# Optimization experiments

Hardware: AMD Instinct MI355X
Metric: run time of the kernel (lower is better)

The kernel has to match this reference:

```python
import jax, jax.numpy as jnp
import numpy as np

N = 50000      # num_nodes
E = 800000     # undirected edge count (maps holds 2E directed maps)
D = 4          # stalk dimension


def setup_inputs() -> dict:
    key = jax.random.key(0)
    k1, k2, k3 = jax.random.split(key, 3)
    maps = jax.random.normal(k1, (2 * E, D, D), dtype=jnp.float32) * 0.3
    # ensure every node appears as a source at least once (avoids degenerate
    # identity eigenproblems for isolated nodes)
    row = jnp.concatenate([jnp.arange(N, dtype=jnp.int32),
                           jax.random.randint(k2, (E - N,), 0, N, dtype=jnp.int32)])
    col = jax.random.randint(k3, (E,), 0, N, dtype=jnp.int32)
    # second half of edge_index is the reversed orientation, as the module assumes
    edge_index = jnp.stack([jnp.concatenate([row, col]),
                            jnp.concatenate([col, row])])
    return {"maps": maps, "edge_index": edge_index, "num_nodes": N}


def reference(maps, edge_index, num_nodes):
    n = num_nodes
    d = maps.shape[1]
    twoE = maps.shape[0]
    Ee = twoE // 2
    row_all = edge_index[0]                                   # [2E]
    # diag contribution: R^T R per directed edge, scatter-added onto source node
    diag_contrib = jnp.einsum('eki,ekj->eij', maps, maps)     # [2E,d,d]
    maps_diag = jnp.zeros((n, d, d), maps.dtype).at[row_all].add(diag_contrib)
    row = edge_index[0, :Ee]
    col = edge_index[1, :Ee]
    # off-diagonal block: R_ij^T R_ji per undirected edge
    maps_triu = jnp.einsum('eki,ekj->eij', maps[:Ee], maps[Ee:])  # [E,d,d]
    # eval-mode augmentation: + I
    to_inv = maps_diag + jnp.eye(d, dtype=maps.dtype)
    evals, evecs = jnp.linalg.eigh(to_inv)                    # batched tiny eigh
    inv_sqrt = jnp.einsum('nik,nk,njk->nij', evecs,
                          jnp.clip(evals, 1e-8, None) ** -0.5, evecs)
    # normalize: D^{-1/2} blocks, clamp to [-1, 1]
    maps_triu = jnp.clip(jnp.einsum('eik,ekl,elj->eij',
                                    inv_sqrt[row], maps_triu, inv_sqrt[col]), -1.0, 1.0)
    maps_diag = jnp.clip(jnp.einsum('nik,nkl,nlj->nij',
                                    inv_sqrt, maps_diag, inv_sqrt), -1.0, 1.0)
    # COO assembly of the (n*d, n*d) sheaf Laplacian
    ar = jnp.arange(d, dtype=jnp.int32)
    A, B = jnp.meshgrid(ar, ar, indexing='ij')                # [d,d]
    node = jnp.arange(n, dtype=jnp.int32)
    diag_rows = (node[:, None, None] * d + A).reshape(-1)
    diag_cols = (node[:, None, None] * d + B).reshape(-1)
    tri_rows_ij = (row[:, None, None] * d + A).reshape(-1)
    tri_cols_ij = (col[:, None, None] * d + B).reshape(-1)
    tri_rows_ji = (col[:, None, None] * d + A).reshape(-1)
    tri_cols_ji = (row[:, None, None] * d + B).reshape(-1)
    rows = jnp.concatenate([diag_rows, tri_rows_ij, tri_rows_ji])
    cols = jnp.concatenate([diag_cols, tri_cols_ij, tri_cols_ji])
    vals = jnp.concatenate([maps_diag.reshape(-1),
                            (-maps_triu).reshape(-1),
                            (-jnp.swapaxes(maps_triu, 1, 2)).reshape(-1)])
    indices = jnp.stack([rows, cols])                         # [2, K]
    return indices, vals
```

## Files before the change

kernel.cpp:

```cpp
#include <hip/hip_runtime.h>

#define DEG_CAP 96

__device__ __forceinline__ void load4x4(const float* __restrict__ p, float m[4][4]) {
    const float4* q = (const float4*)p;
#pragma unroll
    for (int k = 0; k < 4; ++k) {
        float4 v = q[k];
        m[k][0] = v.x; m[k][1] = v.y; m[k][2] = v.z; m[k][3] = v.w;
    }
}

__device__ __forceinline__ void store4x4(float* __restrict__ p, const float m[4][4]) {
    float4* q = (float4*)p;
#pragma unroll
    for (int k = 0; k < 4; ++k)
        q[k] = make_float4(m[k][0], m[k][1], m[k][2], m[k][3]);
}

__device__ __forceinline__ void mmTa(const float a[4][4], const float b[4][4], float o[4][4]) {
#pragma unroll
    for (int i = 0; i < 4; ++i)
#pragma unroll
        for (int j = 0; j < 4; ++j)
            o[i][j] = a[0][i]*b[0][j] + a[1][i]*b[1][j] + a[2][i]*b[2][j] + a[3][i]*b[3][j];
}

__device__ __forceinline__ void mm(const float a[4][4], const float b[4][4], float o[4][4]) {
#pragma unroll
    for (int i = 0; i < 4; ++i)
#pragma unroll
        for (int j = 0; j < 4; ++j)
            o[i][j] = a[i][0]*b[0][j] + a[i][1]*b[1][j] + a[i][2]*b[2][j] + a[i][3]*b[3][j];
}

__global__ void k_fill(const int* __restrict__ ei, int* __restrict__ cnt,
                       int* __restrict__ bucket, int twoE) {
    int e = blockIdx.x * blockDim.x + threadIdx.x;
    if (e >= twoE) return;
    int node = ei[e];
    int slot = atomicAdd(&cnt[(size_t)node * 16], 1);
    if (slot < DEG_CAP)
        bucket[(size_t)node * DEG_CAP + slot] = e;
}

__global__ void k_gather_half(const float* __restrict__ maps, const int* __restrict__ cnt,
                              const int* __restrict__ bucket, float* __restrict__ gram,
                              int N) {
    int tid = blockIdx.x * blockDim.x + threadIdx.x;
    int lane = threadIdx.x & 63;
    int n = (tid >> 6) * 2 + ((lane >> 5) & 1);
    int sub = lane & 31;
    if (n >= N) return;
    int d = cnt[(size_t)n * 16];
    if (d > DEG_CAP) d = DEG_CAP;

    float G[10];
#pragma unroll
    for (int t = 0; t < 10; ++t) G[t] = 0.0f;

#pragma unroll
    for (int rep = 0; rep < 3; ++rep) {
        int slot = sub + rep * 32;
        if (slot < d) {
            int e = bucket[(size_t)n * DEG_CAP + slot];
            float m[4][4];
            load4x4(maps + (size_t)e * 16, m);
            int t = 0;
#pragma unroll
            for (int i = 0; i < 4; ++i)
#pragma unroll
                for (int j = i; j < 4; ++j, ++t)
                    G[t] += m[0][i]*m[0][j] + m[1][i]*m[1][j] + m[2][i]*m[2][j] + m[3][i]*m[3][j];
        }
    }
#pragma unroll
    for (int msk = 1; msk < 32; msk <<= 1) {
#pragma unroll
        for (int t = 0; t < 10; ++t)
            G[t] += __shfl_xor(G[t], msk, 64);
    }
    if (sub == 0) {
        float* g = gram + (size_t)n * 16;
        *(float4*)(g)     = make_float4(G[0], G[1], G[2], G[3]);
        *(float4*)(g + 4) = make_float4(G[4], G[5], G[6], G[7]);
        *(float2*)(g + 8) = make_float2(G[8], G[9]);
    }
}

__global__ void k_diag(const float* __restrict__ gram, float* __restrict__ Rtab,
                       float* __restrict__ out_vals, int N) {
    int n = blockIdx.x * blockDim.x + threadIdx.x;
    if (n >= N) return;
    const float* g = gram + (size_t)n * 16;
    float G[10];
#pragma unroll
    for (int t = 0; t < 10; ++t) G[t] = g[t];
    float D[4][4];
    {
        int t = 0;
#pragma unroll
        for (int i = 0; i < 4; ++i)
#pragma unroll
            for (int j = i; j < 4; ++j, ++t) { D[i][j] = G[t]; D[j][i] = G[t]; }
    }
    float A[4][4], V[4][4];
#pragma unroll
    for (int i = 0; i < 4; ++i)
#pragma unroll
        for (int j = 0; j < 4; ++j) {
            A[i][j] = D[i][j] + (i == j ? 1.0f : 0.0f);
            V[i][j] = (i == j) ? 1.0f : 0.0f;
        }
    const int PP[6] = {0,0,0,1,1,2};
    const int QQ[6] = {1,2,3,2,3,3};
    for (int sweep = 0; sweep < 6; ++sweep) {
        for (int r = 0; r < 6; ++r) {
            int p = PP[r], q = QQ[r];
            float apq = A[p][q];
            if (fabsf(apq) < 1e-12f) continue;
            float tau = (A[q][q] - A[p][p]) / (2.0f * apq);
            float t = copysignf(1.0f, tau) / (fabsf(tau) + sqrtf(1.0f + tau * tau));
            float c = 1.0f / sqrtf(1.0f + t * t);
            float s = t * c;
#pragma unroll
            for (int k = 0; k < 4; ++k) {
                float akp = A[k][p], akq = A[k][q];
                A[k][p] = c * akp - s * akq;
                A[k][q] = s * akp + c * akq;
            }
#pragma unroll
            for (int k = 0; k < 4; ++k) {
                float apk = A[p][k], aqk = A[q][k];
                A[p][k] = c * apk - s * aqk;
                A[q][k] = s * apk + c * aqk;
            }
#pragma unroll
            for (int k = 0; k < 4; ++k) {
                float vkp = V[k][p], vkq = V[k][q];
                V[k][p] = c * vkp - s * vkq;
                V[k][q] = s * vkp + c * vkq;
            }
        }
    }
    float w[4];
#pragma unroll
    for (int k = 0; k < 4; ++k)
        w[k] = 1.0f / sqrtf(fmaxf(A[k][k], 1e-8f));
    float R[4][4];
#pragma unroll
    for (int i = 0; i < 4; ++i)
#pragma unroll
        for (int j = 0; j < 4; ++j)
            R[i][j] = V[i][0]*w[0]*V[j][0] + V[i][1]*w[1]*V[j][1]
                    + V[i][2]*w[2]*V[j][2] + V[i][3]*w[3]*V[j][3];
    store4x4(Rtab + (size_t)n * 16, R);
    float U[4][4], O[4][4];
    mm(R, D, U);
    mm(U, R, O);
#pragma unroll
    for (int i = 0; i < 4; ++i)
#pragma unroll
        for (int j = 0; j < 4; ++j)
            O[i][j] = fminf(fmaxf(O[i][j], -1.0f), 1.0f);
    store4x4(out_vals + (size_t)n * 16, O);
}

__global__ void k_edge_vals(const float* __restrict__ maps, const int* __restrict__ ei,
                            const float* __restrict__ Rtab,
                            float* __restrict__ out_vals, int N, int E) {
    int e = blockIdx.x * blockDim.x + threadIdx.x;
    if (e >= E) return;
    float M1[4][4], M2[4][4];
    load4x4(maps + (size_t)e * 16, M1);
    load4x4(maps + (size_t)(E + e) * 16, M2);
    int r = ei[e];
    int c = ei[2 * E + e];
    float T[4][4];
    mmTa(M1, M2, T);
    float Rr[4][4], Rc[4][4];
    load4x4(Rtab + (size_t)r * 16, Rr);
    load4x4(Rtab + (size_t)c * 16, Rc);
    float U[4][4], S[4][4];
    mm(Rr, T, U);
    mm(U, Rc, S);
#pragma unroll
    for (int i = 0; i < 4; ++i)
#pragma unroll
        for (int j = 0; j < 4; ++j)
            S[i][j] = fminf(fmaxf(S[i][j], -1.0f), 1.0f);

    float4* qv1 = (float4*)(out_vals + (size_t)16 * N + (size_t)e * 16);
    float4* qv2 = (float4*)(out_vals + (size_t)16 * (N + (size_t)E) + (size_t)e * 16);
#pragma unroll
    for (int i = 0; i < 4; ++i) {
        qv1[i] = make_float4(-S[i][0], -S[i][1], -S[i][2], -S[i][3]);
        qv2[i] = make_float4(-S[0][i], -S[1][i], -S[2][i], -S[3][i]);
    }
}

__global__ void k_idx_ij(const int* __restrict__ ei, float* __restrict__ out,
                         size_t Tot, int N, int E) {
    int e = blockIdx.x * blockDim.x + threadIdx.x;
    if (e >= E) return;
    int r = ei[e];
    int c = ei[2 * E + e];
    float rb = (float)(r * 4);
    float cb = (float)(c * 4);
    size_t base = (size_t)16 * N + (size_t)e * 16;
    float4* qr = (float4*)(out + base);
    float4* qc = (float4*)(out + Tot + base);
#pragma unroll
    for (int i = 0; i < 4; ++i) {
        float ri = rb + (float)i;
        qr[i] = make_float4(ri, ri, ri, ri);
        qc[i] = make_float4(cb, cb + 1.0f, cb + 2.0f, cb + 3.0f);
    }
}

__global__ void k_idx_ji(const int* __restrict__ ei, float* __restrict__ out,
                         size_t Tot, int N, int E) {
    int e = blockIdx.x * blockDim.x + threadIdx.x;
    if (e >= E) return;
    int r = ei[e];
    int c = ei[2 * E + e];
    float rb = (float)(r * 4);
    float cb = (float)(c * 4);
    size_t base = (size_t)16 * (N + (size_t)E) + (size_t)e * 16;
    float4* qr = (float4*)(out + base);
    float4* qc = (float4*)(out + Tot + base);
#pragma unroll
    for (int i = 0; i < 4; ++i) {
        float ci = cb + (float)i;
        qr[i] = make_float4(ci, ci, ci, ci);
        qc[i] = make_float4(rb, rb + 1.0f, rb + 2.0f, rb + 3.0f);
    }
}

__global__ void k_nodeB(float* __restrict__ out, size_t Tot, int N) {
    int n = blockIdx.x * blockDim.x + threadIdx.x;
    if (n >= N) return;
    float nb = (float)(n * 4);
    float4* qr = (float4*)(out + (size_t)n * 16);
    float4* qc = (float4*)(out + Tot + (size_t)n * 16);
#pragma unroll
    for (int i = 0; i < 4; ++i) {
        float ni = nb + (float)i;
        qr[i] = make_float4(ni, ni, ni, ni);
        qc[i] = make_float4(nb, nb + 1.0f, nb + 2.0f, nb + 3.0f);
    }
}

extern "C" void kernel_launch(void* const* d_in, const int* in_sizes, int n_in,
                              void* d_out, int out_size, void* d_ws, size_t ws_size,
                              hipStream_t stream) {
    const float* maps = (const float*)d_in[0];
    const int* ei = (const int*)d_in[1];

    int twoE = in_sizes[0] / 16;
    int E = twoE / 2;
    size_t Tot = (size_t)out_size / 3;
    int N = (int)(Tot / 16) - twoE;

    float* out = (float*)d_out;
    float* out_vals = out + 2 * Tot;

    int* bucket = (int*)(out + ((size_t)out_size - (size_t)DEG_CAP * N));
    int* cnt    = (int*)(out + ((size_t)out_size - (size_t)DEG_CAP * N - (size_t)N * 16));
    float* gram =        out + ((size_t)out_size - (size_t)DEG_CAP * N - (size_t)N * 32);
    float* Rtab = out;

    hipMemsetAsync(cnt, 0, (size_t)N * 16 * sizeof(int), stream);

    int bs = 256;
    k_fill<<<(twoE + bs - 1) / bs, bs, 0, stream>>>(ei, cnt, bucket, twoE);
    k_gather_half<<<((size_t)N * 32 + bs - 1) / bs, bs, 0, stream>>>(maps, cnt, bucket, gram, N);
    k_diag<<<(N + bs - 1) / bs, bs, 0, stream>>>(gram, Rtab, out_vals, N);
    k_edge_vals<<<(E + bs - 1) / bs, bs, 0, stream>>>(maps, ei, Rtab, out_vals, N, E);
    k_idx_ij<<<(E + bs - 1) / bs, bs, 0, stream>>>(ei, out, Tot, N, E);
    k_idx_ji<<<(E + bs - 1) / bs, bs, 0, stream>>>(ei, out, Tot, N, E);
    k_nodeB<<<(N + bs - 1) / bs, bs, 0, stream>>>(out, Tot, N);
}
```

Measured before the change: 628.0 us.

## Fuse bucket fill with edge index writes and gram gather with diagonal eigensolve

The edge-index COO writes (both ij and ji orientations) move into the bucket-filling kernel, so edge_index is read once and two launches go away. The per-node gram reduction and the diagonal eigen/inverse-sqrt kernel are merged, which removes the gram workspace round trip and another launch. The catch is that the eigensolve now runs on only one lane of each 32-lane half-wave. That leaves most lanes idle during the heaviest per-node math. The column index is now read from the reversed second half of the source row, which relies on edge_index having the documented mirrored layout.

Measured after the change: 683.4 us. 1.09x slower.

```diff
diff --git a/kernel.cpp b/kernel.cpp
--- a/kernel.cpp
+++ b/kernel.cpp
@@ -34,19 +34,50 @@
             o[i][j] = a[i][0]*b[0][j] + a[i][1]*b[1][j] + a[i][2]*b[2][j] + a[i][3]*b[3][j];
 }
 
-__global__ void k_fill(const int* __restrict__ ei, int* __restrict__ cnt,
-                       int* __restrict__ bucket, int twoE) {
+__global__ void k_fused1(const int* __restrict__ ei, int* __restrict__ cnt,
+                         int* __restrict__ bucket, float* __restrict__ out,
+                         size_t Tot, int N, int E) {
     int e = blockIdx.x * blockDim.x + threadIdx.x;
+    int twoE = 2 * E;
     if (e >= twoE) return;
     int node = ei[e];
     int slot = atomicAdd(&cnt[(size_t)node * 16], 1);
     if (slot < DEG_CAP)
         bucket[(size_t)node * DEG_CAP + slot] = e;
-}
-
-__global__ void k_gather_half(const float* __restrict__ maps, const int* __restrict__ cnt,
-                              const int* __restrict__ bucket, float* __restrict__ gram,
-                              int N) {
+
+    if (e < E) {
+        int r = node;
+        int c = ei[E + e];
+        float rb = (float)(r * 4);
+        float cb = (float)(c * 4);
+        {
+            size_t base = (size_t)16 * N + (size_t)e * 16;
+            float4* qr = (float4*)(out + base);
+            float4* qc = (float4*)(out + Tot + base);
+#pragma unroll
+            for (int i = 0; i < 4; ++i) {
+                float ri = rb + (float)i;
+                qr[i] = make_float4(ri, ri, ri, ri);
+                qc[i] = make_float4(cb, cb + 1.0f, cb + 2.0f, cb + 3.0f);
+            }
+        }
+        {
+            size_t base = (size_t)16 * (N + (size_t)E) + (size_t)e * 16;
+            float4* qr = (float4*)(out + base);
+            float4* qc = (float4*)(out + Tot + base);
+#pragma unroll
+            for (int i = 0; i < 4; ++i) {
+                float ci = cb + (float)i;
+                qr[i] = make_float4(ci, ci, ci, ci);
+                qc[i] = make_float4(rb, rb + 1.0f, rb + 2.0f, rb + 3.0f);
+            }
+        }
+    }
+}
+
+__global__ void k_gather_diag(const float* __restrict__ maps, const int* __restrict__ cnt,
+                              const int* __restrict__ bucket, float* __restrict__ Rtab,
+                              float* __restrict__ out_vals, int N) {
     int tid = blockIdx.x * blockDim.x + threadIdx.x;
     int lane = threadIdx.x & 63;
     int n = (tid >> 6) * 2 + ((lane >> 5) & 1);
@@ -80,22 +111,9 @@
         for (int t = 0; t < 10; ++t)
             G[t] += __shfl_xor(G[t], msk, 64);
     }
-    if (sub == 0) {
-        float* g = gram + (size_t)n * 16;
-        *(float4*)(g)     = make_float4(G[0], G[1], G[2], G[3]);
-        *(float4*)(g + 4) = make_float4(G[4], G[5], G[6], G[7]);
-        *(float2*)(g + 8) = make_float2(G[8], G[9]);
-    }
-}
-
-__global__ void k_diag(const float* __restrict__ gram, float* __restrict__ Rtab,
-                       float* __restrict__ out_vals, int N) {
-    int n = blockIdx.x * blockDim.x + threadIdx.x;
-    if (n >= N) return;
-    const float* g = gram + (size_t)n * 16;
-    float G[10];
-#pragma unroll
-    for (int t = 0; t < 10; ++t) G[t] = g[t];
+
+    if (sub != 0) return;
+
     float D[4][4];
     {
         int t = 0;
@@ -199,44 +217,6 @@
     }
 }
 
-__global__ void k_idx_ij(const int* __restrict__ ei, float* __restrict__ out,
-                         size_t Tot, int N, int E) {
-    int e = blockIdx.x * blockDim.x + threadIdx.x;
-    if (e >= E) return;
-    int r = ei[e];
-    int c = ei[2 * E + e];
-    float rb = (float)(r * 4);
-    float cb = (float)(c * 4);
-    size_t base = (size_t)16 * N + (size_t)e * 16;
-    float4* qr = (float4*)(out + base);
-    float4* qc = (float4*)(out + Tot + base);
-#pragma unroll
-    for (int i = 0; i < 4; ++i) {
-        float ri = rb + (float)i;
-        qr[i] = make_float4(ri, ri, ri, ri);
-        qc[i] = make_float4(cb, cb + 1.0f, cb + 2.0f, cb + 3.0f);
-    }
-}
-
-__global__ void k_idx_ji(const int* __restrict__ ei, float* __restrict__ out,
-                         size_t Tot, int N, int E) {
-    int e = blockIdx.x * blockDim.x + threadIdx.x;
-    if (e >= E) return;
-    int r = ei[e];
-    int c = ei[2 * E + e];
-    float rb = (float)(r * 4);
-    float cb = (float)(c * 4);
-    size_t base = (size_t)16 * (N + (size_t)E) + (size_t)e * 16;
-    float4* qr = (float4*)(out + base);
-    float4* qc = (float4*)(out + Tot + base);
-#pragma unroll
-    for (int i = 0; i < 4; ++i) {
-        float ci = cb + (float)i;
-        qr[i] = make_float4(ci, ci, ci, ci);
-        qc[i] = make_float4(rb, rb + 1.0f, rb + 2.0f, rb + 3.0f);
-    }
-}
-
 __global__ void k_nodeB(float* __restrict__ out, size_t Tot, int N) {
     int n = blockIdx.x * blockDim.x + threadIdx.x;
     if (n >= N) return;
@@ -267,17 +247,13 @@
 
     int* bucket = (int*)(out + ((size_t)out_size - (size_t)DEG_CAP * N));
     int* cnt    = (int*)(out + ((size_t)out_size - (size_t)DEG_CAP * N - (size_t)N * 16));
-    float* gram =        out + ((size_t)out_size - (size_t)DEG_CAP * N - (size_t)N * 32);
     float* Rtab = out;
 
     hipMemsetAsync(cnt, 0, (size_t)N * 16 * sizeof(int), stream);
 
     int bs = 256;
-    k_fill<<<(twoE + bs - 1) / bs, bs, 0, stream>>>(ei, cnt, bucket, twoE);
-    k_gather_half<<<((size_t)N * 32 + bs - 1) / bs, bs, 0, stream>>>(maps, cnt, bucket, gram, N);
-    k_diag<<<(N + bs - 1) / bs, bs, 0, stream>>>(gram, Rtab, out_vals, N);
+    k_fused1<<<(twoE + bs - 1) / bs, bs, 0, stream>>>(ei, cnt, bucket, out, Tot, N, E);
+    k_gather_diag<<<((size_t)N * 32 + bs - 1) / bs, bs, 0, stream>>>(maps, cnt, bucket, Rtab, out_vals, N);
     k_edge_vals<<<(E + bs - 1) / bs, bs, 0, stream>>>(maps, ei, Rtab, out_vals, N, E);
-    k_idx_ij<<<(E + bs - 1) / bs, bs, 0, stream>>>(ei, out, Tot, N, E);
-    k_idx_ji<<<(E + bs - 1) / bs, bs, 0, stream>>>(ei, out, Tot, N, E);
     k_nodeB<<<(N + bs - 1) / bs, bs, 0, stream>>>(out, Tot, N);
 }
```
